# Kernel tuning notes

Hardware: AMD Instinct MI355X
Metric: run time of the kernel (lower is better)

Reference implementation:

```python
import jax, jax.numpy as jnp
import numpy as np

B_, T_, IN_, OUT_, N_ = 16, 4096, 512, 512, 512


def setup_inputs() -> dict:
    key = jax.random.key(0)
    ks = jax.random.split(key, 9)
    u = jax.random.normal(ks[0], (B_, T_, IN_), dtype=jnp.float32)
    # LRU init per original module
    rmin, rmax, max_phase = 0.9, 1.0, 6.283
    u1 = jax.random.uniform(ks[1], (N_,), dtype=jnp.float32)
    u2 = jax.random.uniform(ks[2], (N_,), dtype=jnp.float32)
    nu_log = jnp.log(-0.5 * jnp.log(u1 * (rmax + rmin) * (rmax - rmin) + rmin ** 2))
    theta_log = jnp.log(max_phase * u2)
    Lambda_mod = jnp.exp(-jnp.exp(nu_log))
    gamma_log = jnp.log(jnp.sqrt(1.0 - jnp.square(Lambda_mod)))
    B_re = jax.random.normal(ks[3], (N_, IN_), dtype=jnp.float32) / np.sqrt(2 * IN_)
    B_im = jax.random.normal(ks[4], (N_, IN_), dtype=jnp.float32) / np.sqrt(2 * IN_)
    C_re = jax.random.normal(ks[5], (OUT_, N_), dtype=jnp.float32) / np.sqrt(N_)
    C_im = jax.random.normal(ks[6], (OUT_, N_), dtype=jnp.float32) / np.sqrt(N_)
    D = jax.random.normal(ks[7], (OUT_, IN_), dtype=jnp.float32) / np.sqrt(IN_)
    return {"u": u, "nu_log": nu_log, "theta_log": theta_log, "gamma_log": gamma_log,
            "B_re": B_re, "B_im": B_im, "C_re": C_re, "C_im": C_im, "D": D}


def reference(u, nu_log, theta_log, gamma_log, B_re, B_im, C_re, C_im, D):
    # Lambda: diagonal complex transition, |Lambda| = exp(-exp(nu_log)), angle = exp(theta_log)
    mod = jnp.exp(-jnp.exp(nu_log))             # [N]
    theta = jnp.exp(theta_log)
    Lam = jax.lax.complex(mod * jnp.cos(theta), mod * jnp.sin(theta))  # [N] complex64
    gammas = jnp.exp(gamma_log)                  # [N]
    Bc = jax.lax.complex(B_re, B_im) * gammas[:, None]                 # [N, IN]
    Cc = jax.lax.complex(C_re, C_im)                                   # [OUT, N]

    # input projection: Bu[b,t,n] = sum_i Bc[n,i] * u[b,t,i]
    Bu = jnp.einsum('bti,ni->btn', u.astype(Bc.dtype), Bc)             # [B,T,N] complex

    # diagonal linear recurrence x_t = Lam * x_{t-1} + Bu_t, state starts at 0
    a = jnp.broadcast_to(Lam, Bu.shape)

    def combine(e1, e2):
        a1, b1 = e1
        a2, b2 = e2
        return a1 * a2, a2 * b1 + b2

    _, x = jax.lax.associative_scan(combine, (a, Bu), axis=1)          # x: [B,T,N]

    y = 2.0 * jnp.einsum('btn,on->bto', x, Cc).real + jnp.einsum('bti,oi->bto', u, D)
    return y
```

## Files before the change

### kernel.cpp

```cpp
#include <hip/hip_runtime.h>
#include <hip/hip_bf16.h>
#include <cstdint>
#include <cstddef>


using short8 = __attribute__((ext_vector_type(8))) short;
using f32x4 = __attribute__((ext_vector_type(4))) float;

#define BDIM 16
#define TDIM 4096
#define MTOT (BDIM * TDIM)
#define CHUNK 64
#define NCHUNK (TDIM / CHUNK)

__device__ __forceinline__ unsigned short f2bf(float f) {
    unsigned u = __float_as_uint(f);
    u = u + 0x7FFFu + ((u >> 16) & 1u);
    return (unsigned short)(u >> 16);
}
__device__ __forceinline__ float bflo(unsigned w) { return __uint_as_float(w << 16); }
__device__ __forceinline__ float bfhi(unsigned w) { return __uint_as_float(w & 0xFFFF0000u); }

__device__ __forceinline__ size_t perm_off(int row, int kt, int kp, int rowbytes) {
    int kk = kp >> 5, km = kp & 31;
    int half = km >> 4;
    int g = (km & 15) >> 2, j = km & 3;
    int cc = (kk << 2) | g;
    int c = cc ^ (row & 7);
    return (size_t)row * rowbytes + kt * 128 + (c << 4) + half * 8 + j * 2;
}

__device__ __forceinline__ void gload_lds16(const void* g, void* l) {
    __builtin_amdgcn_global_load_lds((const __attribute__((address_space(1))) void*)g,
                                     (__attribute__((address_space(3))) void*)l, 16, 0, 0);
}

__global__ void prep_w1(const float* __restrict__ B_re, const float* __restrict__ B_im,
                        const float* __restrict__ gamma_log, char* __restrict__ W1) {
    int i = blockIdx.x * 256 + threadIdx.x;
    int r = blockIdx.y;
    int n = r >> 1;
    float gmm = expf(gamma_log[n]);
    float v = (r & 1) ? B_im[n * 512 + i] * gmm : B_re[n * 512 + i] * gmm;
    *(unsigned short*)(W1 + perm_off(r, i >> 6, i & 63, 1024)) = f2bf(v);
}

__global__ void prep_w2(const float* __restrict__ C_re, const float* __restrict__ C_im,
                        const float* __restrict__ D, char* __restrict__ W2) {
    int k = blockIdx.x * 256 + threadIdx.x;
    int o = blockIdx.y;
    float v;
    if (k < 1024) {
        int n = k >> 1;
        v = (k & 1) ? -2.0f * C_im[o * 512 + n] : 2.0f * C_re[o * 512 + n];
    } else {
        v = D[o * 512 + (k - 1024)];
    }
    *(unsigned short*)(W2 + perm_off(o, k >> 6, k & 63, 3072)) = f2bf(v);
}

__global__ void convert_u(const float4* __restrict__ u4, char* __restrict__ Apack) {
    size_t idx = (size_t)blockIdx.x * 256 + threadIdx.x;
    float4 v = u4[idx];
    int row = (int)(idx >> 7);
    int c4 = (int)(idx & 127);
    int kg = 1024 + c4 * 4;
    unsigned lo = (unsigned)f2bf(v.x) | ((unsigned)f2bf(v.y) << 16);
    unsigned hi = (unsigned)f2bf(v.z) | ((unsigned)f2bf(v.w) << 16);
    size_t off = perm_off(row, kg >> 6, kg & 63, 3072);
    *reinterpret_cast<uint2*>(Apack + off) = make_uint2(lo, hi);
}

#define ASM_VMCNT0 asm volatile("s_waitcnt vmcnt(0)" ::: "memory")
#define ASM_LGKM0  asm volatile("s_waitcnt lgkmcnt(0)" ::: "memory")
#define ASM_LGKM2  asm volatile("s_waitcnt lgkmcnt(2)" ::: "memory")
#define ASM_LGKM4  asm volatile("s_waitcnt lgkmcnt(4)" ::: "memory")
#define SCHED0     __builtin_amdgcn_sched_barrier(0)
#define BARRIER    __builtin_amdgcn_s_barrier()
#define PRIO1      __builtin_amdgcn_s_setprio(1)
#define PRIO0      __builtin_amdgcn_s_setprio(0)

template <int OUT_MODE, int NBN, int LDAB, int LDBB>
__global__ __launch_bounds__(512, 2) void gemm_nt(const char* __restrict__ A,
                                                  const char* __restrict__ Bm,
                                                  void* __restrict__ Cout, int ktiles,
                                                  float2* __restrict__ carry,
                                                  const float* __restrict__ nu_log,
                                                  const float* __restrict__ theta_log) {
    __shared__ __align__(16) char lds[131072];
    const int tid = threadIdx.x;
    const int lane = tid & 63, w = tid >> 6;
    const int bid = blockIdx.x;
    const int cpx = gridDim.x >> 3;
    const int swz = (bid & 7) * cpx + (bid >> 3);
    const int bm = swz / NBN, bn = swz % NBN;
    const int wm = (w >> 2) * 128, wn = (w & 3) * 64;
    const int ml = lane & 15, g = lane >> 4;

    const char* AgrL = A + (size_t)(bm * 256 + w * 16 + (lane >> 3)) * LDAB + (lane & 7) * 16;
    const char* BgrL = Bm + (size_t)(bn * 256 + w * 16 + (lane >> 3)) * LDBB + (lane & 7) * 16;

#define STG_A(h, kt_, q) do {                                                         \
        const char* s_ = AgrL + (size_t)((h) * 128) * LDAB + (size_t)(kt_) * 128;     \
        char* d_ = lds + (q) * 65536 + (h) * 16384 + w * 2048;                        \
        gload_lds16(s_, d_);                                                          \
        gload_lds16(s_ + (size_t)8 * LDAB, d_ + 1024);                                \
    } while (0)
#define STG_B(h, kt_, q) do {                                                         \
        const char* s_ = BgrL + (size_t)((h) * 128) * LDBB + (size_t)(kt_) * 128;     \
        char* d_ = lds + (q) * 65536 + 32768 + (h) * 16384 + w * 2048;                \
        gload_lds16(s_, d_);                                                          \
        gload_lds16(s_ + (size_t)8 * LDBB, d_ + 1024);                                \
    } while (0)

#define RD_A1(bank, mt_, Abase) do {                                                  \
        _Pragma("unroll") for (int kk = 0; kk < 2; ++kk) {                            \
            int r_ = wm + (bank) * 64 + (mt_) * 16 + ml;                              \
            int hf_ = r_ >> 7, rl_ = r_ & 127;                                        \
            afr[mt_][kk] = *reinterpret_cast<const short8*>(                          \
                (Abase) + hf_ * 16384 + rl_ * 128 + ((((kk << 2) | g) ^ (rl_ & 7)) << 4)); \
        } } while (0)
#define RD_B1(nh, ntq, Bbase) do {                                                    \
        _Pragma("unroll") for (int kk = 0; kk < 2; ++kk) {                            \
            int c_ = wn + (nh) * 32 + (ntq) * 16 + ml;                                \
            int hf_ = c_ >> 7, cl_ = c_ & 127;                                        \
            bfr[nh][ntq][kk] = *reinterpret_cast<const short8*>(                      \
                (Bbase) + hf_ * 16384 + cl_ * 128 + ((((kk << 2) | g) ^ (cl_ & 7)) << 4)); \
        } } while (0)

#define MFMA8_MT(mh, mtb, nh)                                                         \
    _Pragma("unroll") for (int kk = 0; kk < 2; ++kk)                                  \
    _Pragma("unroll") for (int mi = 0; mi < 2; ++mi)                                  \
    _Pragma("unroll") for (int nt = 0; nt < 2; ++nt)                                  \
        acc[(mh) * 4 + (mtb) + mi][(nh) * 2 + nt] = __builtin_amdgcn_mfma_f32_16x16x32_bf16( \
            afr[(mtb) + mi][kk], bfr[nh][nt][kk], acc[(mh) * 4 + (mtb) + mi][(nh) * 2 + nt], 0, 0, 0)
#define MFMA8_NT(mh, nh, ntq)                                                         \
    _Pragma("unroll") for (int kk = 0; kk < 2; ++kk)                                  \
    _Pragma("unroll") for (int mt = 0; mt < 4; ++mt)                                  \
        acc[(mh) * 4 + mt][(nh) * 2 + (ntq)] = __builtin_amdgcn_mfma_f32_16x16x32_bf16( \
            afr[mt][kk], bfr[nh][ntq][kk], acc[(mh) * 4 + mt][(nh) * 2 + (ntq)], 0, 0, 0)

    f32x4 acc[8][4] = {};
    short8 afr[4][2];
    short8 bfr[2][2][2];

    STG_A(0, 0, 0); STG_A(1, 0, 0); STG_B(0, 0, 0); STG_B(1, 0, 0);
    ASM_VMCNT0;
    BARRIER;

#pragma unroll 2
    for (int kt = 0; kt < ktiles; ++kt) {
        const int cur = kt & 1, nq = cur ^ 1;
        const char* Ab = lds + cur * 65536;
        const char* Bb = Ab + 32768;
        const bool more = (kt + 1 < ktiles);
        RD_B1(0, 0, Bb); RD_B1(0, 1, Bb);
        RD_A1(0, 0, Ab); RD_A1(0, 1, Ab);
        SCHED0;
        RD_A1(0, 2, Ab); RD_A1(0, 3, Ab);
        if (more) { STG_A(0, kt + 1, nq); STG_A(1, kt + 1, nq); }
        ASM_LGKM4; SCHED0;
        PRIO1; MFMA8_MT(0, 0, 0); PRIO0;
        ASM_LGKM0; SCHED0;
        PRIO1; MFMA8_MT(0, 2, 0); PRIO0;
        RD_B1(1, 0, Bb);
        SCHED0;
        RD_B1(1, 1, Bb);
        if (more) { STG_B(0, kt + 1, nq); STG_B(1, kt + 1, nq); }
        ASM_LGKM2; SCHED0;
        PRIO1; MFMA8_NT(0, 1, 0); PRIO0;
        ASM_LGKM0; SCHED0;
        PRIO1; MFMA8_NT(0, 1, 1); PRIO0;
        RD_A1(1, 0, Ab); RD_A1(1, 1, Ab);
        SCHED0;
        RD_A1(1, 2, Ab); RD_A1(1, 3, Ab);
        ASM_LGKM4; SCHED0;
        PRIO1; MFMA8_MT(1, 0, 0); PRIO0;
        ASM_LGKM0; SCHED0;
        PRIO1; MFMA8_MT(1, 2, 0); PRIO0;
        PRIO1; MFMA8_MT(1, 0, 1); MFMA8_MT(1, 2, 1); PRIO0;
        ASM_VMCNT0;
        BARRIER;
    }

    if (OUT_MODE == 0) {
        float* O = (float*)Cout;
#pragma unroll
        for (int mt = 0; mt < 8; ++mt)
#pragma unroll
            for (int nt = 0; nt < 4; ++nt)
#pragma unroll
                for (int r_ = 0; r_ < 4; ++r_) {
                    int grow = bm * 256 + wm + mt * 16 + g * 4 + r_;
                    int gcol = bn * 256 + wn + nt * 16 + ml;
                    O[(size_t)grow * 512 + gcol] = acc[mt][nt][r_];
                }
    } else {
        unsigned short* BuOut = (unsigned short*)Cout;
#pragma unroll
        for (int mt = 0; mt < 8; ++mt)
#pragma unroll
            for (int nt = 0; nt < 4; ++nt)
#pragma unroll
                for (int r_ = 0; r_ < 4; ++r_) {
                    int lrow = wm + mt * 16 + g * 4 + r_;
                    int lcol = wn + nt * 16 + ml;
                    unsigned short hv = f2bf(acc[mt][nt][r_]);
                    *(unsigned short*)(lds + lrow * 512 + lcol * 2) = hv;
                    BuOut[(size_t)(bm * 256 + lrow) * 1024 + bn * 256 + lcol] = hv;
                }
        ASM_LGKM0;
        BARRIER;
        SCHED0;
        int n_local = tid & 127, c_local = tid >> 7;
        int nglob = bn * 128 + n_local;
        float mod = expf(-expf(nu_log[nglob]));
        float th = expf(theta_log[nglob]);
        float s, co;
        sincosf(th, &s, &co);
        float Lre = mod * co, Lim = mod * s;
        const char* base = lds + (c_local * 64) * 512 + n_local * 4;
        float xr = 0.f, xi = 0.f;
#pragma unroll 8
        for (int t = 0; t < 64; ++t) {
            unsigned wv = *reinterpret_cast<const unsigned*>(base + t * 512);
            float nr = fmaf(Lre, xr, fmaf(-Lim, xi, bflo(wv)));
            float ni = fmaf(Lre, xi, fmaf(Lim, xr, bfhi(wv)));
            xr = nr; xi = ni;
        }
        int b = (bm * 256) >> 12;
        int cglob = (((bm * 256) & 4095) >> 6) + c_local;
        carry[(size_t)(b * NCHUNK + cglob) * 512 + nglob] = make_float2(xr, xi);
    }
#undef STG_A
#undef STG_B
#undef RD_A1
#undef RD_B1
#undef MFMA8_MT
#undef MFMA8_NT
}

__global__ void scan_prefix(const float2* __restrict__ carry, const float* __restrict__ nu_log,
                            const float* __restrict__ theta_log, float2* __restrict__ prefix) {
    int q = blockIdx.x * 256 + threadIdx.x;
    int n = q & 511, b = q >> 9;
    float e = expf(nu_log[n]);
    float modL = expf(-(float)CHUNK * e);
    float th = expf(theta_log[n]);
    double ang = fmod((double)CHUNK * (double)th, 6.283185307179586);
    float s, co;
    sincosf((float)ang, &s, &co);
    float Lre = modL * co, Lim = modL * s;
    float pr = 0.f, pi = 0.f;
    for (int c = 0; c < NCHUNK; ++c) {
        size_t idx = (size_t)(b * NCHUNK + c) * 512 + n;
        prefix[idx] = make_float2(pr, pi);
        float2 ev = carry[idx];
        float nr = fmaf(Lre, pr, fmaf(-Lim, pi, ev.x));
        float ni = fmaf(Lre, pi, fmaf(Lim, pr, ev.y));
        pr = nr; pi = ni;
    }
}

__global__ void scan_apply(const unsigned* __restrict__ Bu, const float* __restrict__ nu_log,
                           const float* __restrict__ theta_log, const float2* __restrict__ prefix,
                           char* __restrict__ Apack) {
    int q = blockIdx.x * 256 + threadIdx.x;
    int n = q & 511, c = (q >> 9) & 63, b = q >> 15;
    float mod = expf(-expf(nu_log[n]));
    float th = expf(theta_log[n]);
    float s, co;
    sincosf(th, &s, &co);
    float Lre = mod * co, Lim = mod * s;
    const unsigned* p = Bu + ((size_t)(b * TDIM + c * CHUNK)) * 512 + n;
    float2 pv = prefix[(size_t)(b * NCHUNK + c) * 512 + n];
    float xr = pv.x, xi = pv.y;
    int kp = (2 * n) & 63;
    int kk = kp >> 5, km = kp & 31;
    int half = km >> 4, gg = (km & 15) >> 2, j = km & 3;
    int cc = (kk << 2) | gg;
    int partial = (n >> 5) * 128 + half * 8 + j * 2;
    int row0 = b * TDIM + c * CHUNK;
#pragma unroll 8
    for (int t = 0; t < CHUNK; ++t) {
        unsigned wv = p[(size_t)t * 512];
        float nr = fmaf(Lre, xr, fmaf(-Lim, xi, bflo(wv)));
        float ni = fmaf(Lre, xi, fmaf(Lim, xr, bfhi(wv)));
        xr = nr; xi = ni;
        int row = row0 + t;
        size_t off = (size_t)row * 3072 + ((cc ^ (row & 7)) << 4) + partial;
        *reinterpret_cast<unsigned*>(Apack + off) =
            (unsigned)f2bf(xr) | ((unsigned)f2bf(xi) << 16);
    }
}

extern "C" void kernel_launch(void* const* d_in, const int* in_sizes, int n_in,
                              void* d_out, int out_size, void* d_ws, size_t ws_size,
                              hipStream_t stream) {
    const float* u         = (const float*)d_in[0];
    const float* nu_log    = (const float*)d_in[1];
    const float* theta_log = (const float*)d_in[2];
    const float* gamma_log = (const float*)d_in[3];
    const float* B_re      = (const float*)d_in[4];
    const float* B_im      = (const float*)d_in[5];
    const float* C_re      = (const float*)d_in[6];
    const float* C_im      = (const float*)d_in[7];
    const float* D         = (const float*)d_in[8];

    char* ws = (char*)d_ws;
    char* Apack = ws;
    size_t off = (size_t)MTOT * 3072;
    char* W1 = ws + off; off += 1024 * 1024;
    char* W2 = ws + off; off += 512 * 3072;
    float2* carry  = (float2*)(ws + off); off += (size_t)BDIM * NCHUNK * 512 * 8;
    float2* prefix = (float2*)(ws + off); off += (size_t)BDIM * NCHUNK * 512 * 8;

    unsigned short* Bu = (unsigned short*)d_out;

    prep_w1<<<dim3(2, 1024), 256, 0, stream>>>(B_re, B_im, gamma_log, W1);
    prep_w2<<<dim3(6, 512), 256, 0, stream>>>(C_re, C_im, D, W2);
    convert_u<<<32768, 256, 0, stream>>>((const float4*)u, Apack);
    gemm_nt<1, 4, 3072, 1024><<<1024, 512, 0, stream>>>(Apack + 16 * 128, W1,
                                                        (void*)Bu, 8, carry, nu_log, theta_log);
    scan_prefix<<<32, 256, 0, stream>>>(carry, nu_log, theta_log, prefix);
    scan_apply<<<2048, 256, 0, stream>>>((const unsigned*)Bu, nu_log, theta_log, prefix, Apack);
    gemm_nt<0, 2, 3072, 3072><<<512, 512, 0, stream>>>(Apack, W2, d_out, 24,
                                                       nullptr, nullptr, nullptr);
}
```

Baseline: 300.3 us.

## Load B fragments straight from global into registers, halving LDS staging

The GEMM no longer stages the B operand through LDS. Each wave now loads its B fragments for the next k-tile directly from global memory into registers, overlapping that load with the current tile's MFMAs. The LDS double buffer shrinks to A only, and the vmcnt waits are reworked to allow partial waits. This is meant to cut LDS write/read traffic and the B-related waits inside the loop. In exchange, waves sharing a column block fetch the same B data redundantly from global/L2, register pressure rises, and the loop is no longer unrolled by two.

```diff
diff --git a/kernel.cpp b/kernel.cpp
--- a/kernel.cpp
+++ b/kernel.cpp
@@ -72,8 +72,9 @@
 }
 
 #define ASM_VMCNT0 asm volatile("s_waitcnt vmcnt(0)" ::: "memory")
+#define ASM_VMCNT4 asm volatile("s_waitcnt vmcnt(4)" ::: "memory")
+#define ASM_VMCNT8 asm volatile("s_waitcnt vmcnt(8)" ::: "memory")
 #define ASM_LGKM0  asm volatile("s_waitcnt lgkmcnt(0)" ::: "memory")
-#define ASM_LGKM2  asm volatile("s_waitcnt lgkmcnt(2)" ::: "memory")
 #define ASM_LGKM4  asm volatile("s_waitcnt lgkmcnt(4)" ::: "memory")
 #define SCHED0     __builtin_amdgcn_sched_barrier(0)
 #define BARRIER    __builtin_amdgcn_s_barrier()
@@ -98,89 +99,81 @@
     const int ml = lane & 15, g = lane >> 4;
 
     const char* AgrL = A + (size_t)(bm * 256 + w * 16 + (lane >> 3)) * LDAB + (lane & 7) * 16;
-    const char* BgrL = Bm + (size_t)(bn * 256 + w * 16 + (lane >> 3)) * LDBB + (lane & 7) * 16;
 
 #define STG_A(h, kt_, q) do {                                                         \
         const char* s_ = AgrL + (size_t)((h) * 128) * LDAB + (size_t)(kt_) * 128;     \
-        char* d_ = lds + (q) * 65536 + (h) * 16384 + w * 2048;                        \
+        char* d_ = lds + (q) * 32768 + (h) * 16384 + w * 2048;                        \
         gload_lds16(s_, d_);                                                          \
         gload_lds16(s_ + (size_t)8 * LDAB, d_ + 1024);                                \
     } while (0)
-#define STG_B(h, kt_, q) do {                                                         \
-        const char* s_ = BgrL + (size_t)((h) * 128) * LDBB + (size_t)(kt_) * 128;     \
-        char* d_ = lds + (q) * 65536 + 32768 + (h) * 16384 + w * 2048;                \
-        gload_lds16(s_, d_);                                                          \
-        gload_lds16(s_ + (size_t)8 * LDBB, d_ + 1024);                                \
-    } while (0)
-
-#define RD_A1(bank, mt_, Abase) do {                                                  \
+
+#define LOADB(kt_) do {                                                               \
+        _Pragma("unroll") for (int nh = 0; nh < 2; ++nh)                              \
+        _Pragma("unroll") for (int ntq = 0; ntq < 2; ++ntq)                           \
         _Pragma("unroll") for (int kk = 0; kk < 2; ++kk) {                            \
-            int r_ = wm + (bank) * 64 + (mt_) * 16 + ml;                              \
+            int c_ = bn * 256 + wn + nh * 32 + ntq * 16 + ml;                         \
+            bfr[nh][ntq][kk] = *reinterpret_cast<const short8*>(                      \
+                Bm + (size_t)c_ * LDBB + (size_t)(kt_) * 128 +                        \
+                ((((kk << 2) | g) ^ (ml & 7)) << 4));                                 \
+        } } while (0)
+
+#define RD_A1(mh, mt_, Abase) do {                                                    \
+        _Pragma("unroll") for (int kk = 0; kk < 2; ++kk) {                            \
+            int r_ = wm + (mh) * 64 + (mt_) * 16 + ml;                                \
             int hf_ = r_ >> 7, rl_ = r_ & 127;                                        \
             afr[mt_][kk] = *reinterpret_cast<const short8*>(                          \
                 (Abase) + hf_ * 16384 + rl_ * 128 + ((((kk << 2) | g) ^ (rl_ & 7)) << 4)); \
         } } while (0)
-#define RD_B1(nh, ntq, Bbase) do {                                                    \
-        _Pragma("unroll") for (int kk = 0; kk < 2; ++kk) {                            \
-            int c_ = wn + (nh) * 32 + (ntq) * 16 + ml;                                \
-            int hf_ = c_ >> 7, cl_ = c_ & 127;                                        \
-            bfr[nh][ntq][kk] = *reinterpret_cast<const short8*>(                      \
-                (Bbase) + hf_ * 16384 + cl_ * 128 + ((((kk << 2) | g) ^ (cl_ & 7)) << 4)); \
-        } } while (0)
-
-#define MFMA8_MT(mh, mtb, nh)                                                         \
+
+#define MFMA16_MT(mh, mtb)                                                            \
     _Pragma("unroll") for (int kk = 0; kk < 2; ++kk)                                  \
     _Pragma("unroll") for (int mi = 0; mi < 2; ++mi)                                  \
+    _Pragma("unroll") for (int nh = 0; nh < 2; ++nh)                                  \
     _Pragma("unroll") for (int nt = 0; nt < 2; ++nt)                                  \
-        acc[(mh) * 4 + (mtb) + mi][(nh) * 2 + nt] = __builtin_amdgcn_mfma_f32_16x16x32_bf16( \
-            afr[(mtb) + mi][kk], bfr[nh][nt][kk], acc[(mh) * 4 + (mtb) + mi][(nh) * 2 + nt], 0, 0, 0)
-#define MFMA8_NT(mh, nh, ntq)                                                         \
-    _Pragma("unroll") for (int kk = 0; kk < 2; ++kk)                                  \
-    _Pragma("unroll") for (int mt = 0; mt < 4; ++mt)                                  \
-        acc[(mh) * 4 + mt][(nh) * 2 + (ntq)] = __builtin_amdgcn_mfma_f32_16x16x32_bf16( \
-            afr[mt][kk], bfr[nh][ntq][kk], acc[(mh) * 4 + mt][(nh) * 2 + (ntq)], 0, 0, 0)
+        acc[(mh) * 4 + (mtb) + mi][nh * 2 + nt] = __builtin_amdgcn_mfma_f32_16x16x32_bf16( \
+            afr[(mtb) + mi][kk], bfr[nh][nt][kk], acc[(mh) * 4 + (mtb) + mi][nh * 2 + nt], 0, 0, 0)
 
     f32x4 acc[8][4] = {};
     short8 afr[4][2];
     short8 bfr[2][2][2];
 
-    STG_A(0, 0, 0); STG_A(1, 0, 0); STG_B(0, 0, 0); STG_B(1, 0, 0);
-    ASM_VMCNT0;
+    STG_A(0, 0, 0); STG_A(1, 0, 0);
+    LOADB(0);
+    ASM_VMCNT8;
     BARRIER;
-
-#pragma unroll 2
+    SCHED0;
+
     for (int kt = 0; kt < ktiles; ++kt) {
         const int cur = kt & 1, nq = cur ^ 1;
-        const char* Ab = lds + cur * 65536;
-        const char* Bb = Ab + 32768;
+        const char* Ab = lds + cur * 32768;
         const bool more = (kt + 1 < ktiles);
-        RD_B1(0, 0, Bb); RD_B1(0, 1, Bb);
+        if (more) {
+            STG_A(0, kt + 1, nq); STG_A(1, kt + 1, nq);
+            ASM_VMCNT4;
+        } else {
+            ASM_VMCNT0;
+        }
+        SCHED0;
         RD_A1(0, 0, Ab); RD_A1(0, 1, Ab);
         SCHED0;
         RD_A1(0, 2, Ab); RD_A1(0, 3, Ab);
-        if (more) { STG_A(0, kt + 1, nq); STG_A(1, kt + 1, nq); }
         ASM_LGKM4; SCHED0;
-        PRIO1; MFMA8_MT(0, 0, 0); PRIO0;
+        PRIO1; MFMA16_MT(0, 0); PRIO0;
         ASM_LGKM0; SCHED0;
-        PRIO1; MFMA8_MT(0, 2, 0); PRIO0;
-        RD_B1(1, 0, Bb);
-        SCHED0;
-        RD_B1(1, 1, Bb);
-        if (more) { STG_B(0, kt + 1, nq); STG_B(1, kt + 1, nq); }
-        ASM_LGKM2; SCHED0;
-        PRIO1; MFMA8_NT(0, 1, 0); PRIO0;
-        ASM_LGKM0; SCHED0;
-        PRIO1; MFMA8_NT(0, 1, 1); PRIO0;
+        PRIO1; MFMA16_MT(0, 2); PRIO0;
         RD_A1(1, 0, Ab); RD_A1(1, 1, Ab);
         SCHED0;
         RD_A1(1, 2, Ab); RD_A1(1, 3, Ab);
         ASM_LGKM4; SCHED0;
-        PRIO1; MFMA8_MT(1, 0, 0); PRIO0;
+        PRIO1; MFMA16_MT(1, 0); PRIO0;
         ASM_LGKM0; SCHED0;
-        PRIO1; MFMA8_MT(1, 2, 0); PRIO0;
-        PRIO1; MFMA8_MT(1, 0, 1); MFMA8_MT(1, 2, 1); PRIO0;
-        ASM_VMCNT0;
+        PRIO1; MFMA16_MT(1, 2); PRIO0;
+        if (more) {
+            LOADB(kt + 1);
+            ASM_VMCNT8;
+        }
         BARRIER;
+        SCHED0;
     }
 
     if (OUT_MODE == 0) {
@@ -233,11 +226,9 @@
         carry[(size_t)(b * NCHUNK + cglob) * 512 + nglob] = make_float2(xr, xi);
     }
 #undef STG_A
-#undef STG_B
+#undef LOADB
 #undef RD_A1
-#undef RD_B1
-#undef MFMA8_MT
-#undef MFMA8_NT
+#undef MFMA16_MT
 }
 
 __global__ void scan_prefix(const float2* __restrict__ carry, const float* __restrict__ nu_log,
```

Result: slower. 337.9 us (+12.5%).
